# Performance work log

Hardware: AMD Instinct MI355X
Metric: run time of the kernel (lower is better)

Reference implementation:

```python
import jax, jax.numpy as jnp
import numpy as np

B, H, S, D = 4, 16, 2048, 64

def setup_inputs() -> dict:
    key = jax.random.key(0)
    kq, kk, kv, km = jax.random.split(key, 4)
    encodings_q = jax.random.normal(kq, (B, H, S, D), dtype=jnp.float32)
    encodings_k = jax.random.normal(kk, (B, H, S, D), dtype=jnp.float32)
    encodings_v = jax.random.normal(kv, (B, H, S, D), dtype=jnp.float32)
    mask = jax.random.randint(km, (B, 1, S, S), 0, 2).astype(jnp.bool_)
    return {"encodings_q": encodings_q, "encodings_k": encodings_k,
            "encodings_v": encodings_v, "mask": mask}

def reference(encodings_q, encodings_k, encodings_v, mask):
    # scaled dot-product attention: softmax(QK^T / sqrt(d) + mask) V
    d = encodings_q.shape[-1]
    scale = 1.0 / jnp.sqrt(jnp.asarray(d, dtype=encodings_q.dtype))
    # [B,H,S,S]
    scores = jnp.einsum('bhqd,bhkd->bhqk', encodings_q, encodings_k) * scale
    neg_inf = jnp.asarray(-1e9, dtype=scores.dtype)
    scores = jnp.where(mask, scores, neg_inf)  # True = keep, False = mask out
    attn = jax.nn.softmax(scores, axis=-1)
    out = jnp.einsum('bhqk,bhkd->bhqd', attn, encodings_v)
    return out
```

## Files before the change

### kernel.cpp

```cpp
#include <hip/hip_runtime.h>
#include <hip/hip_bf16.h>

#define B_ 4
#define H_ 16
#define S_ 2048
#define D_ 64
#define KBLK 64
#define NT (S_/KBLK)

typedef __attribute__((ext_vector_type(16))) float f32x16;
typedef __attribute__((ext_vector_type(4)))  unsigned int u32x4;
typedef __attribute__((ext_vector_type(8)))  short s16x8;
typedef __attribute__((ext_vector_type(8)))  __bf16 bf16x8;
typedef unsigned int u32;

__device__ __forceinline__ unsigned short f2bf(float f) {
    u32 u = __builtin_bit_cast(u32, f);
    u += 0x7FFFu + ((u >> 16) & 1u);
    return (unsigned short)(u >> 16);
}
__device__ __forceinline__ s16x8 cvt8(float4 a, float4 b) {
    s16x8 f;
    f[0] = (short)f2bf(a.x); f[1] = (short)f2bf(a.y);
    f[2] = (short)f2bf(a.z); f[3] = (short)f2bf(a.w);
    f[4] = (short)f2bf(b.x); f[5] = (short)f2bf(b.y);
    f[6] = (short)f2bf(b.z); f[7] = (short)f2bf(b.w);
    return f;
}
__device__ __forceinline__ f32x16 mfma32(s16x8 a, s16x8 b, f32x16 c) {
    return __builtin_amdgcn_mfma_f32_32x32x16_bf16(
        __builtin_bit_cast(bf16x8, a), __builtin_bit_cast(bf16x8, b), c, 0, 0, 0);
}
__device__ __forceinline__ void gll16(const void* g, void* l) {
    __builtin_amdgcn_global_load_lds(
        (const __attribute__((address_space(1))) unsigned int*)g,
        (__attribute__((address_space(3))) unsigned int*)l, 16, 0, 0);
}
__device__ __forceinline__ u32 pkcvt(float lo, float hi) {
    u32 r;
    asm("v_cvt_pk_bf16_f32 %0, %1, %2" : "=v"(r) : "v"(lo), "v"(hi));
    return r;
}
__device__ __forceinline__ float fand(float x, u32 m) {
    return __builtin_bit_cast(float, __builtin_bit_cast(u32, x) & m);
}

__global__ __launch_bounds__(256) void prep_kv(const float* __restrict__ K,
                                               const float* __restrict__ V,
                                               short* __restrict__ Kb,
                                               short* __restrict__ VT) {
    __shared__ float tile[64][65];
    const int bh = blockIdx.y;
    const int kc = blockIdx.x * 64;
    const int t = threadIdx.x;

    {
        const int r = t >> 2, c = (t & 3) * 16;
        const float* src = K + ((size_t)bh * S_ + kc + r) * D_ + c;
        float4 a0 = *(const float4*)(src + 0);
        float4 a1 = *(const float4*)(src + 4);
        float4 a2 = *(const float4*)(src + 8);
        float4 a3 = *(const float4*)(src + 12);
        short* dst = Kb + ((size_t)bh * S_ + kc + r) * D_ + c;
        *(s16x8*)dst       = cvt8(a0, a1);
        *(s16x8*)(dst + 8) = cvt8(a2, a3);
    }

    const float* src = V + (size_t)bh * S_ * D_ + (size_t)kc * D_;
#pragma unroll
    for (int p = 0; p < 4; ++p) {
        int idx = p * 256 + t;
        int r = idx >> 4;
        int c = (idx & 15) * 4;
        float4 v = *(const float4*)(src + (size_t)r * D_ + c);
        tile[r][c+0] = v.x; tile[r][c+1] = v.y; tile[r][c+2] = v.z; tile[r][c+3] = v.w;
    }
    __syncthreads();
    const int d = t >> 2, c0 = (t & 3) * 16;
    s16x8 o0, o1;
#pragma unroll
    for (int j = 0; j < 8; ++j) {
        o0[j] = (short)f2bf(tile[c0 + j][d]);
        o1[j] = (short)f2bf(tile[c0 + 8 + j][d]);
    }
    short* dst = VT + (size_t)bh * D_ * S_ + (size_t)d * S_ + kc + c0;
    *(s16x8*)dst = o0;
    *(s16x8*)(dst + 8) = o1;
}

__global__ __launch_bounds__(256) void mk_pairs(const int* __restrict__ M,
                                                u32* __restrict__ PM) {
    const u32 gid = blockIdx.x * 256 + threadIdx.x;
    const int w = gid & 15;
    const int q = (gid >> 4) & 2047;
    const int t = (gid >> 15) & 31;
    const int b = gid >> 20;
    const int k = t * 64 + ((w >> 2) & 1) * 32 + 8 * (w & 3) + 4 * (w >> 3);

    const int4 a = *(const int4*)(M + (((size_t)b * S_ + q) * S_ + k));
    PM[gid] = (a.x ? 0xFFu : 0u) | (a.y ? 0xFF00u : 0u) |
              (a.z ? 0xFF0000u : 0u) | (a.w ? 0xFF000000u : 0u);
}

__global__ __launch_bounds__(256) void attn_fwd(
    const float* __restrict__ Q, const short* __restrict__ Kb,
    const short* __restrict__ VTb, const u32* __restrict__ PM,
    float* __restrict__ O)
{
    __shared__ short kbuf[2][KBLK * D_];
    __shared__ short vbuf[2][KBLK * D_];

    const int tid = threadIdx.x;
    const int w  = tid >> 6;
    const int l  = tid & 63;
    const int ql = l & 31;
    const int h  = l >> 5;
    const int m7 = l & 7;

    const int dd    = blockIdx.x;
    const int xcd   = dd & 7;
    const int slot  = dd >> 3;
    const int bh    = xcd * 8 + (slot >> 4);
    const int qtile = slot & 15;
    const int b     = bh >> 4;
    const int qrow  = qtile * 128 + w * 32 + ql;

    const float* Qp  = Q   + (size_t)bh * S_ * D_;
    const short* Kp  = Kb  + (size_t)bh * S_ * D_;
    const short* Vp  = VTb + (size_t)bh * D_ * S_;
    const u32*   pmp = PM  + (((size_t)b * NT) * S_ + qrow) * 16 + h * 8;
    float* Op = O + (size_t)bh * S_ * D_;

    const float qscale = 0.125f * 1.44269504088896f;
    s16x8 qfrag[4];
#pragma unroll
    for (int ks = 0; ks < 4; ++ks) {
        const float* src = Qp + (size_t)qrow * D_ + ks * 16 + h * 8;
        float4 a = *(const float4*)(src);
        float4 c = *(const float4*)(src + 4);
        float4 as = make_float4(a.x*qscale, a.y*qscale, a.z*qscale, a.w*qscale);
        float4 cs = make_float4(c.x*qscale, c.y*qscale, c.z*qscale, c.w*qscale);
        qfrag[ks] = cvt8(as, cs);
    }

    int offs[2][4];
#pragma unroll
    for (int bk = 0; bk < 2; ++bk)
#pragma unroll
        for (int ks = 0; ks < 4; ++ks)
            offs[bk][ks] = (bk * 32 + ql) * 128 + (((ks * 2 + h) ^ m7) << 4);

    const int srow = w * 16 + (l >> 3);
    const int sg   = m7 ^ (l >> 3);
    const char* KsrcB = (const char*)Kp + (size_t)srow * 128 + sg * 16;
    const char* VsrcB = (const char*)Vp + (size_t)srow * (S_ * 2) + sg * 16;

    f32x16 oacc0 = (f32x16)(0.f), oacc1 = (f32x16)(0.f);
    float lh = 0.f;

    {
        short* kd = &kbuf[0][(w * 16) * 64];
        short* vd = &vbuf[0][(w * 16) * 64];
        gll16(KsrcB,            kd);
        gll16(KsrcB + 1024,     kd + 8 * 64);
        gll16(VsrcB,            vd);
        gll16(VsrcB + 8 * 4096, vd + 8 * 64);
    }
    u32x4 bmn0 = *(const u32x4*)(pmp);
    u32x4 bmn1 = *(const u32x4*)(pmp + 4);

    for (int t = 0; t < NT; ++t) {
        const int cur = t & 1;
        asm volatile("s_waitcnt vmcnt(0)" ::: "memory");
        __syncthreads();
        if (t + 1 < NT) {
            short* kd = &kbuf[cur ^ 1][(w * 16) * 64];
            short* vd = &vbuf[cur ^ 1][(w * 16) * 64];
            gll16(KsrcB + (size_t)(t + 1) * 8192,           kd);
            gll16(KsrcB + (size_t)(t + 1) * 8192 + 1024,    kd + 8 * 64);
            gll16(VsrcB + (size_t)(t + 1) * 128,            vd);
            gll16(VsrcB + (size_t)(t + 1) * 128 + 8 * 4096, vd + 8 * 64);
        }

        const u32x4 bmc0 = bmn0, bmc1 = bmn1;
        if (t + 1 < NT) {
            const u32* pmt = pmp + (size_t)(t + 1) * (S_ * 16);
            bmn0 = *(const u32x4*)(pmt);
            bmn1 = *(const u32x4*)(pmt + 4);
        }

        const char* kbp = (const char*)kbuf[cur];
        f32x16 s0 = (f32x16)(0.f), s1 = (f32x16)(0.f);
#pragma unroll
        for (int ks = 0; ks < 4; ++ks)
            s0 = mfma32(*(const s16x8*)(kbp + offs[0][ks]), qfrag[ks], s0);
#pragma unroll
        for (int ks = 0; ks < 4; ++ks)
            s1 = mfma32(*(const s16x8*)(kbp + offs[1][ks]), qfrag[ks], s1);

        float ps = 0.f;
        u32 pk0[8], pk1[8];
#pragma unroll
        for (int j = 0; j < 8; ++j) {
            const u32 word = bmc0[j >> 1];
            const u32 mlo = (j & 1) ? (u32)(((int)(word <<  8)) >> 24)
                                    : (u32)(((int)(word << 24)) >> 24);
            const u32 mhi = (j & 1) ? (u32)(((int)word) >> 24)
                                    : (u32)(((int)(word << 16)) >> 24);
            float a0 = fand(__builtin_amdgcn_exp2f(s0[2*j]),   mlo);
            float a1 = fand(__builtin_amdgcn_exp2f(s0[2*j+1]), mhi);
            ps += a0 + a1;
            pk0[j] = pkcvt(a0, a1);
        }
#pragma unroll
        for (int j = 0; j < 8; ++j) {
            const u32 word = bmc1[j >> 1];
            const u32 mlo = (j & 1) ? (u32)(((int)(word <<  8)) >> 24)
                                    : (u32)(((int)(word << 24)) >> 24);
            const u32 mhi = (j & 1) ? (u32)(((int)word) >> 24)
                                    : (u32)(((int)(word << 16)) >> 24);
            float a0 = fand(__builtin_amdgcn_exp2f(s1[2*j]),   mlo);
            float a1 = fand(__builtin_amdgcn_exp2f(s1[2*j+1]), mhi);
            ps += a0 + a1;
            pk1[j] = pkcvt(a0, a1);
        }
        lh += ps;

        asm("v_permlane32_swap_b32 %0, %1" : "+v"(pk0[0]), "+v"(pk0[2]));
        asm("v_permlane32_swap_b32 %0, %1" : "+v"(pk0[1]), "+v"(pk0[3]));
        asm("v_permlane32_swap_b32 %0, %1" : "+v"(pk0[4]), "+v"(pk0[6]));
        asm("v_permlane32_swap_b32 %0, %1" : "+v"(pk0[5]), "+v"(pk0[7]));
        asm("v_permlane32_swap_b32 %0, %1" : "+v"(pk1[0]), "+v"(pk1[2]));
        asm("v_permlane32_swap_b32 %0, %1" : "+v"(pk1[1]), "+v"(pk1[3]));
        asm("v_permlane32_swap_b32 %0, %1" : "+v"(pk1[4]), "+v"(pk1[6]));
        asm("v_permlane32_swap_b32 %0, %1" : "+v"(pk1[5]), "+v"(pk1[7]));

        s16x8 pfrag[4];
        {
            u32x4 f0 = {pk0[0], pk0[1], pk0[2], pk0[3]};
            u32x4 f1 = {pk0[4], pk0[5], pk0[6], pk0[7]};
            u32x4 f2 = {pk1[0], pk1[1], pk1[2], pk1[3]};
            u32x4 f3 = {pk1[4], pk1[5], pk1[6], pk1[7]};
            pfrag[0] = __builtin_bit_cast(s16x8, f0);
            pfrag[1] = __builtin_bit_cast(s16x8, f1);
            pfrag[2] = __builtin_bit_cast(s16x8, f2);
            pfrag[3] = __builtin_bit_cast(s16x8, f3);
        }

        const char* vbp = (const char*)vbuf[cur];
#pragma unroll
        for (int ks = 0; ks < 4; ++ks) {
            oacc0 = mfma32(*(const s16x8*)(vbp + offs[0][ks]), pfrag[ks], oacc0);
            oacc1 = mfma32(*(const s16x8*)(vbp + offs[1][ks]), pfrag[ks], oacc1);
        }
    }

    lh += __shfl_xor(lh, 32);
    const float inv = 1.0f / lh;
#pragma unroll
    for (int rg = 0; rg < 4; ++rg) {
        float4 st;
        st.x = oacc0[rg*4+0] * inv; st.y = oacc0[rg*4+1] * inv;
        st.z = oacc0[rg*4+2] * inv; st.w = oacc0[rg*4+3] * inv;
        *(float4*)(Op + (size_t)qrow * D_ + rg * 8 + h * 4) = st;
        float4 su;
        su.x = oacc1[rg*4+0] * inv; su.y = oacc1[rg*4+1] * inv;
        su.z = oacc1[rg*4+2] * inv; su.w = oacc1[rg*4+3] * inv;
        *(float4*)(Op + (size_t)qrow * D_ + 32 + rg * 8 + h * 4) = su;
    }
}

extern "C" void kernel_launch(void* const* d_in, const int* in_sizes, int n_in,
                              void* d_out, int out_size, void* d_ws, size_t ws_size,
                              hipStream_t stream) {
    const float* Q = (const float*)d_in[0];
    const float* K = (const float*)d_in[1];
    const float* V = (const float*)d_in[2];
    const int*   M = (const int*)d_in[3];
    float* O = (float*)d_out;
    (void)in_sizes; (void)n_in; (void)out_size; (void)ws_size;

    char* ws = (char*)d_ws;
    short* Kb  = (short*)(ws);
    short* VTb = (short*)(ws + 16777216);
    u32*   PM  = (u32*)  (ws + 33554432);

    prep_kv <<<dim3(S_ / 64, B_ * H_), 256, 0, stream>>>(K, V, Kb, VTb);
    mk_pairs<<<16384, 256, 0, stream>>>(M, PM);
    attn_fwd<<<1024, 256, 0, stream>>>(Q, Kb, VTb, PM, O);
}
```

Before: 137.5 us.

## Shrink key block to 32 and query tile to 64 with two-wave blocks

Halves the key block per iteration from 64 to 32 and the query tile per workgroup from 128 to 64, launching 2048 blocks of 128 threads instead of 1024 of 256. The mask packing, LDS swizzles and staging offsets are rewritten for the new 32-key, 64-row V^T layout, and the next-tile prefetch is issued after the QK MFMAs. The aim is higher occupancy, a smaller LDS footprint and lower register pressure per wave. In exchange it runs twice as many loop iterations and barriers, and each K/V tile is reused by fewer query rows.

```diff
diff --git a/kernel.cpp b/kernel.cpp
--- a/kernel.cpp
+++ b/kernel.cpp
@@ -5,7 +5,7 @@
 #define H_ 16
 #define S_ 2048
 #define D_ 64
-#define KBLK 64
+#define KBLK 32
 #define NT (S_/KBLK)
 
 typedef __attribute__((ext_vector_type(16))) float f32x16;
@@ -91,44 +91,43 @@
 __global__ __launch_bounds__(256) void mk_pairs(const int* __restrict__ M,
                                                 u32* __restrict__ PM) {
     const u32 gid = blockIdx.x * 256 + threadIdx.x;
-    const int w = gid & 15;
-    const int q = (gid >> 4) & 2047;
-    const int t = (gid >> 15) & 31;
+    const int w = gid & 7;
+    const int q = (gid >> 3) & 2047;
+    const int t = (gid >> 14) & 63;
     const int b = gid >> 20;
-    const int k = t * 64 + ((w >> 2) & 1) * 32 + 8 * (w & 3) + 4 * (w >> 3);
+    const int k = t * 32 + 8 * (w & 3) + 4 * (w >> 2);
 
     const int4 a = *(const int4*)(M + (((size_t)b * S_ + q) * S_ + k));
     PM[gid] = (a.x ? 0xFFu : 0u) | (a.y ? 0xFF00u : 0u) |
               (a.z ? 0xFF0000u : 0u) | (a.w ? 0xFF000000u : 0u);
 }
 
-__global__ __launch_bounds__(256) void attn_fwd(
+__global__ __launch_bounds__(128) void attn_fwd(
     const float* __restrict__ Q, const short* __restrict__ Kb,
     const short* __restrict__ VTb, const u32* __restrict__ PM,
     float* __restrict__ O)
 {
     __shared__ short kbuf[2][KBLK * D_];
-    __shared__ short vbuf[2][KBLK * D_];
+    __shared__ short vbuf[2][D_ * KBLK];
 
     const int tid = threadIdx.x;
     const int w  = tid >> 6;
     const int l  = tid & 63;
     const int ql = l & 31;
     const int h  = l >> 5;
-    const int m7 = l & 7;
 
     const int dd    = blockIdx.x;
     const int xcd   = dd & 7;
     const int slot  = dd >> 3;
-    const int bh    = xcd * 8 + (slot >> 4);
-    const int qtile = slot & 15;
+    const int bh    = xcd * 8 + (slot >> 5);
+    const int qtile = slot & 31;
     const int b     = bh >> 4;
-    const int qrow  = qtile * 128 + w * 32 + ql;
+    const int qrow  = qtile * 64 + w * 32 + ql;
 
     const float* Qp  = Q   + (size_t)bh * S_ * D_;
     const short* Kp  = Kb  + (size_t)bh * S_ * D_;
     const short* Vp  = VTb + (size_t)bh * D_ * S_;
-    const u32*   pmp = PM  + (((size_t)b * NT) * S_ + qrow) * 16 + h * 8;
+    const u32*   pmp = PM  + (((size_t)b * NT) * S_ + qrow) * 8 + h * 4;
     float* Op = O + (size_t)bh * S_ * D_;
 
     const float qscale = 0.125f * 1.44269504088896f;
@@ -143,66 +142,67 @@
         qfrag[ks] = cvt8(as, cs);
     }
 
-    int offs[2][4];
-#pragma unroll
-    for (int bk = 0; bk < 2; ++bk)
-#pragma unroll
-        for (int ks = 0; ks < 4; ++ks)
-            offs[bk][ks] = (bk * 32 + ql) * 128 + (((ks * 2 + h) ^ m7) << 4);
-
-    const int srow = w * 16 + (l >> 3);
-    const int sg   = m7 ^ (l >> 3);
-    const char* KsrcB = (const char*)Kp + (size_t)srow * 128 + sg * 16;
-    const char* VsrcB = (const char*)Vp + (size_t)srow * (S_ * 2) + sg * 16;
+    int offsK[4];
+#pragma unroll
+    for (int ks = 0; ks < 4; ++ks)
+        offsK[ks] = ql * 128 + (((ks * 2 + h) ^ (ql & 7)) << 4);
+    int offsV[2][2];
+#pragma unroll
+    for (int dt = 0; dt < 2; ++dt)
+#pragma unroll
+        for (int ks = 0; ks < 2; ++ks)
+            offsV[dt][ks] = (dt * 32 + ql) * 64 + (((ks * 2 + h) ^ (ql & 3)) << 4);
+
+    const int srowK = tid >> 3;
+    const int sgK   = (tid & 7) ^ (srowK & 7);
+    const char* KsrcB = (const char*)Kp + (size_t)srowK * 128 + sgK * 16;
+    const int srowV = tid >> 2;
+    const int sgV   = (tid & 3) ^ (srowV & 3);
+    const char* VsrcB = (const char*)Vp + (size_t)srowV * (S_ * 2) + sgV * 16;
 
     f32x16 oacc0 = (f32x16)(0.f), oacc1 = (f32x16)(0.f);
     float lh = 0.f;
 
     {
-        short* kd = &kbuf[0][(w * 16) * 64];
-        short* vd = &vbuf[0][(w * 16) * 64];
-        gll16(KsrcB,            kd);
-        gll16(KsrcB + 1024,     kd + 8 * 64);
-        gll16(VsrcB,            vd);
-        gll16(VsrcB + 8 * 4096, vd + 8 * 64);
-    }
-    u32x4 bmn0 = *(const u32x4*)(pmp);
-    u32x4 bmn1 = *(const u32x4*)(pmp + 4);
+        short* kd = &kbuf[0][w * 512];
+        gll16(KsrcB,                       kd);
+        gll16(KsrcB + 16 * 128,            kd + 1024);
+        short* vd = &vbuf[0][w * 512];
+        gll16(VsrcB,                       vd);
+        gll16(VsrcB + (size_t)32 * S_ * 2, vd + 1024);
+    }
+    u32x4 bmn = *(const u32x4*)(pmp);
 
     for (int t = 0; t < NT; ++t) {
         const int cur = t & 1;
         asm volatile("s_waitcnt vmcnt(0)" ::: "memory");
         __syncthreads();
+
+        const u32x4 bmc = bmn;
+
+        const char* kbp = (const char*)kbuf[cur];
+        f32x16 s0 = (f32x16)(0.f);
+#pragma unroll
+        for (int ks = 0; ks < 4; ++ks)
+            s0 = mfma32(*(const s16x8*)(kbp + offsK[ks]), qfrag[ks], s0);
+
         if (t + 1 < NT) {
-            short* kd = &kbuf[cur ^ 1][(w * 16) * 64];
-            short* vd = &vbuf[cur ^ 1][(w * 16) * 64];
-            gll16(KsrcB + (size_t)(t + 1) * 8192,           kd);
-            gll16(KsrcB + (size_t)(t + 1) * 8192 + 1024,    kd + 8 * 64);
-            gll16(VsrcB + (size_t)(t + 1) * 128,            vd);
-            gll16(VsrcB + (size_t)(t + 1) * 128 + 8 * 4096, vd + 8 * 64);
-        }
-
-        const u32x4 bmc0 = bmn0, bmc1 = bmn1;
-        if (t + 1 < NT) {
-            const u32* pmt = pmp + (size_t)(t + 1) * (S_ * 16);
-            bmn0 = *(const u32x4*)(pmt);
-            bmn1 = *(const u32x4*)(pmt + 4);
-        }
-
-        const char* kbp = (const char*)kbuf[cur];
-        f32x16 s0 = (f32x16)(0.f), s1 = (f32x16)(0.f);
-#pragma unroll
-        for (int ks = 0; ks < 4; ++ks)
-            s0 = mfma32(*(const s16x8*)(kbp + offs[0][ks]), qfrag[ks], s0);
-#pragma unroll
-        for (int ks = 0; ks < 4; ++ks)
-            s1 = mfma32(*(const s16x8*)(kbp + offs[1][ks]), qfrag[ks], s1);
+            short* kd = &kbuf[cur ^ 1][w * 512];
+            const char* ks2 = KsrcB + (size_t)(t + 1) * (KBLK * 128);
+            gll16(ks2,            kd);
+            gll16(ks2 + 16 * 128, kd + 1024);
+            short* vd = &vbuf[cur ^ 1][w * 512];
+            const char* vs2 = VsrcB + (size_t)(t + 1) * (KBLK * 2);
+            gll16(vs2,                       vd);
+            gll16(vs2 + (size_t)32 * S_ * 2, vd + 1024);
+            bmn = *(const u32x4*)(pmp + (size_t)(t + 1) * (S_ * 8));
+        }
 
         float ps = 0.f;
-        u32 pk0[8], pk1[8];
+        u32 pk0[8];
 #pragma unroll
         for (int j = 0; j < 8; ++j) {
-            const u32 word = bmc0[j >> 1];
+            const u32 word = bmc[j >> 1];
             const u32 mlo = (j & 1) ? (u32)(((int)(word <<  8)) >> 24)
                                     : (u32)(((int)(word << 24)) >> 24);
             const u32 mhi = (j & 1) ? (u32)(((int)word) >> 24)
@@ -212,46 +212,26 @@
             ps += a0 + a1;
             pk0[j] = pkcvt(a0, a1);
         }
-#pragma unroll
-        for (int j = 0; j < 8; ++j) {
-            const u32 word = bmc1[j >> 1];
-            const u32 mlo = (j & 1) ? (u32)(((int)(word <<  8)) >> 24)
-                                    : (u32)(((int)(word << 24)) >> 24);
-            const u32 mhi = (j & 1) ? (u32)(((int)word) >> 24)
-                                    : (u32)(((int)(word << 16)) >> 24);
-            float a0 = fand(__builtin_amdgcn_exp2f(s1[2*j]),   mlo);
-            float a1 = fand(__builtin_amdgcn_exp2f(s1[2*j+1]), mhi);
-            ps += a0 + a1;
-            pk1[j] = pkcvt(a0, a1);
-        }
         lh += ps;
 
         asm("v_permlane32_swap_b32 %0, %1" : "+v"(pk0[0]), "+v"(pk0[2]));
         asm("v_permlane32_swap_b32 %0, %1" : "+v"(pk0[1]), "+v"(pk0[3]));
         asm("v_permlane32_swap_b32 %0, %1" : "+v"(pk0[4]), "+v"(pk0[6]));
         asm("v_permlane32_swap_b32 %0, %1" : "+v"(pk0[5]), "+v"(pk0[7]));
-        asm("v_permlane32_swap_b32 %0, %1" : "+v"(pk1[0]), "+v"(pk1[2]));
-        asm("v_permlane32_swap_b32 %0, %1" : "+v"(pk1[1]), "+v"(pk1[3]));
-        asm("v_permlane32_swap_b32 %0, %1" : "+v"(pk1[4]), "+v"(pk1[6]));
-        asm("v_permlane32_swap_b32 %0, %1" : "+v"(pk1[5]), "+v"(pk1[7]));
-
-        s16x8 pfrag[4];
+
+        s16x8 pfrag[2];
         {
             u32x4 f0 = {pk0[0], pk0[1], pk0[2], pk0[3]};
             u32x4 f1 = {pk0[4], pk0[5], pk0[6], pk0[7]};
-            u32x4 f2 = {pk1[0], pk1[1], pk1[2], pk1[3]};
-            u32x4 f3 = {pk1[4], pk1[5], pk1[6], pk1[7]};
             pfrag[0] = __builtin_bit_cast(s16x8, f0);
             pfrag[1] = __builtin_bit_cast(s16x8, f1);
-            pfrag[2] = __builtin_bit_cast(s16x8, f2);
-            pfrag[3] = __builtin_bit_cast(s16x8, f3);
         }
 
         const char* vbp = (const char*)vbuf[cur];
 #pragma unroll
-        for (int ks = 0; ks < 4; ++ks) {
-            oacc0 = mfma32(*(const s16x8*)(vbp + offs[0][ks]), pfrag[ks], oacc0);
-            oacc1 = mfma32(*(const s16x8*)(vbp + offs[1][ks]), pfrag[ks], oacc1);
+        for (int ks = 0; ks < 2; ++ks) {
+            oacc0 = mfma32(*(const s16x8*)(vbp + offsV[0][ks]), pfrag[ks], oacc0);
+            oacc1 = mfma32(*(const s16x8*)(vbp + offsV[1][ks]), pfrag[ks], oacc1);
         }
     }
 
@@ -287,5 +267,5 @@
 
     prep_kv <<<dim3(S_ / 64, B_ * H_), 256, 0, stream>>>(K, V, Kb, VTb);
     mk_pairs<<<16384, 256, 0, stream>>>(M, PM);
-    attn_fwd<<<1024, 256, 0, stream>>>(Q, Kb, VTb, PM, O);
-}
+    attn_fwd<<<2048, 128, 0, stream>>>(Q, Kb, VTb, PM, O);
+}
```

Result: slower. 149.5 us (+8.7%).

## Process two query tiles per block to reuse K/V shared tiles

Applied to the files above, without the earlier changes.

Each block now handles 256 query rows (two 128-row sub-tiles A and B) instead of 128, so every K/V tile loaded into shared memory serves twice as many queries. The grid is halved to 512 blocks. The loop body is split into helper functions and interleaves QK, softmax-pack and PV for both sub-tiles, issuing the next tile's prefetch after the first QK so the loads overlap compute. The cost is more registers per thread (two sets of accumulators and Q fragments) and fewer blocks to fill the 256 CUs, which may reduce occupancy and latency hiding.

```diff
diff --git a/kernel.cpp b/kernel.cpp
--- a/kernel.cpp
+++ b/kernel.cpp
@@ -102,6 +102,76 @@
               (a.z ? 0xFF0000u : 0u) | (a.w ? 0xFF000000u : 0u);
 }
 
+__device__ __forceinline__ void qk_pair(const char* kbp, const int offs[2][4],
+                                        const s16x8* qf, f32x16& s0, f32x16& s1) {
+    s0 = (f32x16)(0.f); s1 = (f32x16)(0.f);
+#pragma unroll
+    for (int ks = 0; ks < 4; ++ks)
+        s0 = mfma32(*(const s16x8*)(kbp + offs[0][ks]), qf[ks], s0);
+#pragma unroll
+    for (int ks = 0; ks < 4; ++ks)
+        s1 = mfma32(*(const s16x8*)(kbp + offs[1][ks]), qf[ks], s1);
+}
+
+__device__ __forceinline__ void sm_pack(const f32x16 s0, const f32x16 s1,
+                                        const u32x4 bmc0, const u32x4 bmc1,
+                                        float& lh, s16x8* pfrag) {
+    float ps = 0.f;
+    u32 pk0[8], pk1[8];
+#pragma unroll
+    for (int j = 0; j < 8; ++j) {
+        const u32 word = bmc0[j >> 1];
+        const u32 mlo = (j & 1) ? (u32)(((int)(word <<  8)) >> 24)
+                                : (u32)(((int)(word << 24)) >> 24);
+        const u32 mhi = (j & 1) ? (u32)(((int)word) >> 24)
+                                : (u32)(((int)(word << 16)) >> 24);
+        float a0 = fand(__builtin_amdgcn_exp2f(s0[2*j]),   mlo);
+        float a1 = fand(__builtin_amdgcn_exp2f(s0[2*j+1]), mhi);
+        ps += a0 + a1;
+        pk0[j] = pkcvt(a0, a1);
+    }
+#pragma unroll
+    for (int j = 0; j < 8; ++j) {
+        const u32 word = bmc1[j >> 1];
+        const u32 mlo = (j & 1) ? (u32)(((int)(word <<  8)) >> 24)
+                                : (u32)(((int)(word << 24)) >> 24);
+        const u32 mhi = (j & 1) ? (u32)(((int)word) >> 24)
+                                : (u32)(((int)(word << 16)) >> 24);
+        float a0 = fand(__builtin_amdgcn_exp2f(s1[2*j]),   mlo);
+        float a1 = fand(__builtin_amdgcn_exp2f(s1[2*j+1]), mhi);
+        ps += a0 + a1;
+        pk1[j] = pkcvt(a0, a1);
+    }
+    lh += ps;
+
+    asm("v_permlane32_swap_b32 %0, %1" : "+v"(pk0[0]), "+v"(pk0[2]));
+    asm("v_permlane32_swap_b32 %0, %1" : "+v"(pk0[1]), "+v"(pk0[3]));
+    asm("v_permlane32_swap_b32 %0, %1" : "+v"(pk0[4]), "+v"(pk0[6]));
+    asm("v_permlane32_swap_b32 %0, %1" : "+v"(pk0[5]), "+v"(pk0[7]));
+    asm("v_permlane32_swap_b32 %0, %1" : "+v"(pk1[0]), "+v"(pk1[2]));
+    asm("v_permlane32_swap_b32 %0, %1" : "+v"(pk1[1]), "+v"(pk1[3]));
+    asm("v_permlane32_swap_b32 %0, %1" : "+v"(pk1[4]), "+v"(pk1[6]));
+    asm("v_permlane32_swap_b32 %0, %1" : "+v"(pk1[5]), "+v"(pk1[7]));
+
+    u32x4 f0 = {pk0[0], pk0[1], pk0[2], pk0[3]};
+    u32x4 f1 = {pk0[4], pk0[5], pk0[6], pk0[7]};
+    u32x4 f2 = {pk1[0], pk1[1], pk1[2], pk1[3]};
+    u32x4 f3 = {pk1[4], pk1[5], pk1[6], pk1[7]};
+    pfrag[0] = __builtin_bit_cast(s16x8, f0);
+    pfrag[1] = __builtin_bit_cast(s16x8, f1);
+    pfrag[2] = __builtin_bit_cast(s16x8, f2);
+    pfrag[3] = __builtin_bit_cast(s16x8, f3);
+}
+
+__device__ __forceinline__ void pv_pair(const char* vbp, const int offs[2][4],
+                                        const s16x8* pfrag, f32x16& o0, f32x16& o1) {
+#pragma unroll
+    for (int ks = 0; ks < 4; ++ks) {
+        o0 = mfma32(*(const s16x8*)(vbp + offs[0][ks]), pfrag[ks], o0);
+        o1 = mfma32(*(const s16x8*)(vbp + offs[1][ks]), pfrag[ks], o1);
+    }
+}
+
 __global__ __launch_bounds__(256) void attn_fwd(
     const float* __restrict__ Q, const short* __restrict__ Kb,
     const short* __restrict__ VTb, const u32* __restrict__ PM,
@@ -120,27 +190,35 @@
     const int dd    = blockIdx.x;
     const int xcd   = dd & 7;
     const int slot  = dd >> 3;
-    const int bh    = xcd * 8 + (slot >> 4);
-    const int qtile = slot & 15;
+    const int bh    = xcd * 8 + (slot >> 3);
+    const int qtile = slot & 7;
     const int b     = bh >> 4;
-    const int qrow  = qtile * 128 + w * 32 + ql;
+    const int qrowA = qtile * 256 + w * 32 + ql;
+    const int qrowB = qrowA + 128;
 
     const float* Qp  = Q   + (size_t)bh * S_ * D_;
     const short* Kp  = Kb  + (size_t)bh * S_ * D_;
     const short* Vp  = VTb + (size_t)bh * D_ * S_;
-    const u32*   pmp = PM  + (((size_t)b * NT) * S_ + qrow) * 16 + h * 8;
+    const u32*   pmpA = PM + (((size_t)b * NT) * S_ + qrowA) * 16 + h * 8;
+    const u32*   pmpB = PM + (((size_t)b * NT) * S_ + qrowB) * 16 + h * 8;
     float* Op = O + (size_t)bh * S_ * D_;
 
     const float qscale = 0.125f * 1.44269504088896f;
-    s16x8 qfrag[4];
+    s16x8 qfA[4], qfB[4];
 #pragma unroll
     for (int ks = 0; ks < 4; ++ks) {
-        const float* src = Qp + (size_t)qrow * D_ + ks * 16 + h * 8;
-        float4 a = *(const float4*)(src);
-        float4 c = *(const float4*)(src + 4);
+        const float* srcA = Qp + (size_t)qrowA * D_ + ks * 16 + h * 8;
+        float4 a = *(const float4*)(srcA);
+        float4 c = *(const float4*)(srcA + 4);
         float4 as = make_float4(a.x*qscale, a.y*qscale, a.z*qscale, a.w*qscale);
         float4 cs = make_float4(c.x*qscale, c.y*qscale, c.z*qscale, c.w*qscale);
-        qfrag[ks] = cvt8(as, cs);
+        qfA[ks] = cvt8(as, cs);
+        const float* srcB = Qp + (size_t)qrowB * D_ + ks * 16 + h * 8;
+        float4 a2 = *(const float4*)(srcB);
+        float4 c2 = *(const float4*)(srcB + 4);
+        float4 as2 = make_float4(a2.x*qscale, a2.y*qscale, a2.z*qscale, a2.w*qscale);
+        float4 cs2 = make_float4(c2.x*qscale, c2.y*qscale, c2.z*qscale, c2.w*qscale);
+        qfB[ks] = cvt8(as2, cs2);
     }
 
     int offs[2][4];
@@ -155,8 +233,9 @@
     const char* KsrcB = (const char*)Kp + (size_t)srow * 128 + sg * 16;
     const char* VsrcB = (const char*)Vp + (size_t)srow * (S_ * 2) + sg * 16;
 
-    f32x16 oacc0 = (f32x16)(0.f), oacc1 = (f32x16)(0.f);
-    float lh = 0.f;
+    f32x16 oA0 = (f32x16)(0.f), oA1 = (f32x16)(0.f);
+    f32x16 oB0 = (f32x16)(0.f), oB1 = (f32x16)(0.f);
+    float lhA = 0.f, lhB = 0.f;
 
     {
         short* kd = &kbuf[0][(w * 16) * 64];
@@ -166,13 +245,24 @@
         gll16(VsrcB,            vd);
         gll16(VsrcB + 8 * 4096, vd + 8 * 64);
     }
-    u32x4 bmn0 = *(const u32x4*)(pmp);
-    u32x4 bmn1 = *(const u32x4*)(pmp + 4);
+    u32x4 bmnA0 = *(const u32x4*)(pmpA);
+    u32x4 bmnA1 = *(const u32x4*)(pmpA + 4);
+    u32x4 bmnB0 = *(const u32x4*)(pmpB);
+    u32x4 bmnB1 = *(const u32x4*)(pmpB + 4);
 
     for (int t = 0; t < NT; ++t) {
         const int cur = t & 1;
         asm volatile("s_waitcnt vmcnt(0)" ::: "memory");
         __syncthreads();
+
+        const u32x4 bmcA0 = bmnA0, bmcA1 = bmnA1;
+        const u32x4 bmcB0 = bmnB0, bmcB1 = bmnB1;
+        const char* kbp = (const char*)kbuf[cur];
+        const char* vbp = (const char*)vbuf[cur];
+
+        f32x16 sA0, sA1;
+        qk_pair(kbp, offs, qfA, sA0, sA1);
+
         if (t + 1 < NT) {
             short* kd = &kbuf[cur ^ 1][(w * 16) * 64];
             short* vd = &vbuf[cur ^ 1][(w * 16) * 64];
@@ -180,93 +270,49 @@
             gll16(KsrcB + (size_t)(t + 1) * 8192 + 1024,    kd + 8 * 64);
             gll16(VsrcB + (size_t)(t + 1) * 128,            vd);
             gll16(VsrcB + (size_t)(t + 1) * 128 + 8 * 4096, vd + 8 * 64);
+            const u32* pA = pmpA + (size_t)(t + 1) * (S_ * 16);
+            const u32* pB = pmpB + (size_t)(t + 1) * (S_ * 16);
+            bmnA0 = *(const u32x4*)(pA);
+            bmnA1 = *(const u32x4*)(pA + 4);
+            bmnB0 = *(const u32x4*)(pB);
+            bmnB1 = *(const u32x4*)(pB + 4);
         }
 
-        const u32x4 bmc0 = bmn0, bmc1 = bmn1;
-        if (t + 1 < NT) {
-            const u32* pmt = pmp + (size_t)(t + 1) * (S_ * 16);
-            bmn0 = *(const u32x4*)(pmt);
-            bmn1 = *(const u32x4*)(pmt + 4);
-        }
-
-        const char* kbp = (const char*)kbuf[cur];
-        f32x16 s0 = (f32x16)(0.f), s1 = (f32x16)(0.f);
-#pragma unroll
-        for (int ks = 0; ks < 4; ++ks)
-            s0 = mfma32(*(const s16x8*)(kbp + offs[0][ks]), qfrag[ks], s0);
-#pragma unroll
-        for (int ks = 0; ks < 4; ++ks)
-            s1 = mfma32(*(const s16x8*)(kbp + offs[1][ks]), qfrag[ks], s1);
-
-        float ps = 0.f;
-        u32 pk0[8], pk1[8];
-#pragma unroll
-        for (int j = 0; j < 8; ++j) {
-            const u32 word = bmc0[j >> 1];
-            const u32 mlo = (j & 1) ? (u32)(((int)(word <<  8)) >> 24)
-                                    : (u32)(((int)(word << 24)) >> 24);
-            const u32 mhi = (j & 1) ? (u32)(((int)word) >> 24)
-                                    : (u32)(((int)(word << 16)) >> 24);
-            float a0 = fand(__builtin_amdgcn_exp2f(s0[2*j]),   mlo);
-            float a1 = fand(__builtin_amdgcn_exp2f(s0[2*j+1]), mhi);
-            ps += a0 + a1;
-            pk0[j] = pkcvt(a0, a1);
-        }
-#pragma unroll
-        for (int j = 0; j < 8; ++j) {
-            const u32 word = bmc1[j >> 1];
-            const u32 mlo = (j & 1) ? (u32)(((int)(word <<  8)) >> 24)
-                                    : (u32)(((int)(word << 24)) >> 24);
-            const u32 mhi = (j & 1) ? (u32)(((int)word) >> 24)
-                                    : (u32)(((int)(word << 16)) >> 24);
-            float a0 = fand(__builtin_amdgcn_exp2f(s1[2*j]),   mlo);
-            float a1 = fand(__builtin_amdgcn_exp2f(s1[2*j+1]), mhi);
-            ps += a0 + a1;
-            pk1[j] = pkcvt(a0, a1);
-        }
-        lh += ps;
-
-        asm("v_permlane32_swap_b32 %0, %1" : "+v"(pk0[0]), "+v"(pk0[2]));
-        asm("v_permlane32_swap_b32 %0, %1" : "+v"(pk0[1]), "+v"(pk0[3]));
-        asm("v_permlane32_swap_b32 %0, %1" : "+v"(pk0[4]), "+v"(pk0[6]));
-        asm("v_permlane32_swap_b32 %0, %1" : "+v"(pk0[5]), "+v"(pk0[7]));
-        asm("v_permlane32_swap_b32 %0, %1" : "+v"(pk1[0]), "+v"(pk1[2]));
-        asm("v_permlane32_swap_b32 %0, %1" : "+v"(pk1[1]), "+v"(pk1[3]));
-        asm("v_permlane32_swap_b32 %0, %1" : "+v"(pk1[4]), "+v"(pk1[6]));
-        asm("v_permlane32_swap_b32 %0, %1" : "+v"(pk1[5]), "+v"(pk1[7]));
-
-        s16x8 pfrag[4];
-        {
-            u32x4 f0 = {pk0[0], pk0[1], pk0[2], pk0[3]};
-            u32x4 f1 = {pk0[4], pk0[5], pk0[6], pk0[7]};
-            u32x4 f2 = {pk1[0], pk1[1], pk1[2], pk1[3]};
-            u32x4 f3 = {pk1[4], pk1[5], pk1[6], pk1[7]};
-            pfrag[0] = __builtin_bit_cast(s16x8, f0);
-            pfrag[1] = __builtin_bit_cast(s16x8, f1);
-            pfrag[2] = __builtin_bit_cast(s16x8, f2);
-            pfrag[3] = __builtin_bit_cast(s16x8, f3);
-        }
-
-        const char* vbp = (const char*)vbuf[cur];
-#pragma unroll
-        for (int ks = 0; ks < 4; ++ks) {
-            oacc0 = mfma32(*(const s16x8*)(vbp + offs[0][ks]), pfrag[ks], oacc0);
-            oacc1 = mfma32(*(const s16x8*)(vbp + offs[1][ks]), pfrag[ks], oacc1);
-        }
-    }
-
-    lh += __shfl_xor(lh, 32);
-    const float inv = 1.0f / lh;
+        s16x8 pfA[4];
+        sm_pack(sA0, sA1, bmcA0, bmcA1, lhA, pfA);
+
+        f32x16 sB0, sB1;
+        qk_pair(kbp, offs, qfB, sB0, sB1);
+
+        s16x8 pfB[4];
+        sm_pack(sB0, sB1, bmcB0, bmcB1, lhB, pfB);
+
+        pv_pair(vbp, offs, pfA, oA0, oA1);
+        pv_pair(vbp, offs, pfB, oB0, oB1);
+    }
+
+    lhA += __shfl_xor(lhA, 32);
+    lhB += __shfl_xor(lhB, 32);
+    const float invA = 1.0f / lhA;
+    const float invB = 1.0f / lhB;
 #pragma unroll
     for (int rg = 0; rg < 4; ++rg) {
         float4 st;
-        st.x = oacc0[rg*4+0] * inv; st.y = oacc0[rg*4+1] * inv;
-        st.z = oacc0[rg*4+2] * inv; st.w = oacc0[rg*4+3] * inv;
-        *(float4*)(Op + (size_t)qrow * D_ + rg * 8 + h * 4) = st;
+        st.x = oA0[rg*4+0] * invA; st.y = oA0[rg*4+1] * invA;
+        st.z = oA0[rg*4+2] * invA; st.w = oA0[rg*4+3] * invA;
+        *(float4*)(Op + (size_t)qrowA * D_ + rg * 8 + h * 4) = st;
         float4 su;
-        su.x = oacc1[rg*4+0] * inv; su.y = oacc1[rg*4+1] * inv;
-        su.z = oacc1[rg*4+2] * inv; su.w = oacc1[rg*4+3] * inv;
-        *(float4*)(Op + (size_t)qrow * D_ + 32 + rg * 8 + h * 4) = su;
+        su.x = oA1[rg*4+0] * invA; su.y = oA1[rg*4+1] * invA;
+        su.z = oA1[rg*4+2] * invA; su.w = oA1[rg*4+3] * invA;
+        *(float4*)(Op + (size_t)qrowA * D_ + 32 + rg * 8 + h * 4) = su;
+        float4 sb;
+        sb.x = oB0[rg*4+0] * invB; sb.y = oB0[rg*4+1] * invB;
+        sb.z = oB0[rg*4+2] * invB; sb.w = oB0[rg*4+3] * invB;
+        *(float4*)(Op + (size_t)qrowB * D_ + rg * 8 + h * 4) = sb;
+        float4 sv;
+        sv.x = oB1[rg*4+0] * invB; sv.y = oB1[rg*4+1] * invB;
+        sv.z = oB1[rg*4+2] * invB; sv.w = oB1[rg*4+3] * invB;
+        *(float4*)(Op + (size_t)qrowB * D_ + 32 + rg * 8 + h * 4) = sv;
     }
 }
 
@@ -287,5 +333,5 @@
 
     prep_kv <<<dim3(S_ / 64, B_ * H_), 256, 0, stream>>>(K, V, Kb, VTb);
     mk_pairs<<<16384, 256, 0, stream>>>(M, PM);
-    attn_fwd<<<1024, 256, 0, stream>>>(Q, Kb, VTb, PM, O);
-}
+    attn_fwd<<<512, 256, 0, stream>>>(Q, Kb, VTb, PM, O);
+}
```

Result: slower. 164.4 us (+19.6%).
